# Optimization experiments

Hardware: AMD Instinct MI355X
Metric: run time of the kernel (lower is better)

The kernel has to match this reference:

```python
import jax, jax.numpy as jnp
import numpy as np

IMG = 224      # img_size
P = 16         # patch_size
C = 3          # in_chans
K = 100        # n_segments
COMPACT = 10.0 # slic compactness
ITERS = 10     # slic k-means iterations


def _resize_matrix(src, dst):
    # Linear antialiased resize is a linear map; materialize it by resizing identity.
    return jax.image.resize(jnp.eye(src, dtype=jnp.float32), (dst, src),
                            method='linear', antialias=True)


def _slic_labels(img_hwc):
    """Simplified SLIC: grid-initialized k-means in (color, compactness-scaled xy) space."""
    H, W = IMG, IMG
    S = float(np.sqrt(H * W / K))         # superpixel spacing
    ratio = COMPACT / S                   # spatial scaling (SLIC distance weighting)
    yy, xx = jnp.meshgrid(jnp.arange(H, dtype=jnp.float32),
                          jnp.arange(W, dtype=jnp.float32), indexing='ij')
    feat = jnp.concatenate([img_hwc, (yy * ratio)[..., None], (xx * ratio)[..., None]],
                           axis=-1).reshape(H * W, C + 2)  # [HW, 5]
    # grid init of K centers
    gh = int(np.ceil(np.sqrt(K)))
    gw = int(np.ceil(K / gh))
    cy = ((np.arange(gh) + 0.5) * H / gh).astype(np.int32)
    cx = ((np.arange(gw) + 0.5) * W / gw).astype(np.int32)
    idx = (cy[:, None] * W + cx[None, :]).reshape(-1)[:K]
    centers0 = feat[jnp.asarray(idx)]  # [K, 5]

    f2 = jnp.sum(feat * feat, axis=1, keepdims=True)  # [HW,1]

    def dists(centers):
        c2 = jnp.sum(centers * centers, axis=1)  # [K]
        return f2 + c2[None, :] - 2.0 * (feat @ centers.T)  # [HW,K]

    def body(i, centers):
        lbl = jnp.argmin(dists(centers), axis=1)              # [HW]
        oh = jax.nn.one_hot(lbl, K, dtype=feat.dtype)         # [HW,K]
        cnt = oh.sum(0)                                       # [K]
        new = (oh.T @ feat) / jnp.maximum(cnt, 1.0)[:, None]  # [K,5]
        return jnp.where((cnt > 0)[:, None], new, centers)

    centers = jax.lax.fori_loop(0, ITERS, body, centers0)
    return jnp.argmin(dists(centers), axis=1).reshape(H, W)


def _embed_one(img_chw, A):
    img = jnp.transpose(img_chw, (1, 2, 0))                     # [H,W,C]
    labels = jax.lax.stop_gradient(_slic_labels(img))           # [H,W] int
    masks = jax.nn.one_hot(labels, K, dtype=img.dtype, axis=0)  # [K,H,W]
    masked = masks[..., None] * img[None]                       # [K,H,W,C]
    tmp = jnp.einsum('ph,khwc->kpwc', A, masked)                # resize rows
    return jnp.einsum('qw,kpwc->kpqc', A, tmp)                  # [K,P,P,C]


def reference(x):
    B = x.shape[0]
    A = _resize_matrix(IMG, P)
    sp = jax.vmap(lambda im: _embed_one(im, A))(x)  # [B,K,P,P,C]
    # torch: view(B, K*C, P, P)  (raw row-major reinterpret), flatten(2), transpose(1,2)
    out = sp.reshape(B, K * C, P, P).reshape(B, K * C, P * P)
    return jnp.transpose(out, (0, 2, 1))  # [B, P*P, K*C]


def setup_inputs() -> dict:
    key = jax.random.key(0)
    x = jax.random.uniform(key, (8, C, IMG, IMG), dtype=jnp.float32)
    return {"x": x}
```

## Files before the change

kernel.cpp:

```cpp
#include <hip/hip_runtime.h>
#include <math.h>

#define IMGD 224
#define HW 50176
#define NK 100
#define NB 8
#define OUT_PER_B 76800
#define NCHUNK 131


static __device__ __forceinline__ float ratio_f32() {
  return (float)(10.0 / sqrt(224.0 * 224.0 / 100.0));
}

static __device__ __forceinline__ float dist5s(float f0, float f1, float f2,
                                               float f3, float f4, float fsq,
                                               float c0, float c1, float c2,
                                               float c3, float c4, float q) {
  float dot = __fmul_rn(f0, c0);
  dot = __fmaf_rn(f1, c1, dot);
  dot = __fmaf_rn(f2, c2, dot);
  dot = __fmaf_rn(f3, c3, dot);
  dot = __fmaf_rn(f4, c4, dot);
  return __fsub_rn(__fadd_rn(fsq, q), __fmul_rn(2.0f, dot));
}

static __device__ __forceinline__ float fsq5(float f0, float f1, float f2,
                                             float f3, float f4) {
  float s = __fmul_rn(f0, f0);
  s = __fadd_rn(s, __fmul_rn(f1, f1));
  s = __fadd_rn(s, __fmul_rn(f2, f2));
  s = __fadd_rn(s, __fmul_rn(f3, f3));
  s = __fadd_rn(s, __fmul_rn(f4, f4));
  return s;
}

__global__ void __launch_bounds__(256) setup_kernel(
    const float* __restrict__ x, float* __restrict__ A,
    float* __restrict__ centers, float* __restrict__ c2g) {
  int blk = blockIdx.x;
  int tid = threadIdx.x;
  if (blk < 16) {
    __shared__ float red[256];
    int p = blk;
    float tri = 0.0f;
    if (tid < IMGD) {
      float center = (p + 0.5f) * 14.0f - 0.5f;
      float xd = fabsf(center - (float)tid) / 14.0f;
      tri = fmaxf(0.0f, 1.0f - xd);
    }
    red[tid] = tri;
    __syncthreads();
    for (int s = 128; s > 0; s >>= 1) {
      if (tid < s) red[tid] += red[tid + s];
      __syncthreads();
    }
    float Z = red[0];
    if (tid < IMGD) A[p * IMGD + tid] = tri / Z;
  } else {
    int b = blk - 16;
    int k = tid;
    if (k >= NK) return;
    int gy = k / 10, gx = k % 10;
    int cy = (int)((gy + 0.5) * 224.0 / 10.0);
    int cx = (int)((gx + 0.5) * 224.0 / 10.0);
    int i = cy * IMGD + cx;
    const float ratio = ratio_f32();
    float c0 = x[((size_t)b * 3 + 0) * HW + i];
    float c1 = x[((size_t)b * 3 + 1) * HW + i];
    float c2 = x[((size_t)b * 3 + 2) * HW + i];
    float c3 = __fmul_rn((float)cy, ratio);
    float c4 = __fmul_rn((float)cx, ratio);
    float* c = centers + ((size_t)b * NK + k) * 5;
    c[0] = c0; c[1] = c1; c[2] = c2; c[3] = c3; c[4] = c4;
    float s = __fmul_rn(c0, c0);
    s = __fadd_rn(s, __fmul_rn(c1, c1));
    s = __fadd_rn(s, __fmul_rn(c2, c2));
    s = __fadd_rn(s, __fmul_rn(c3, c3));
    s = __fadd_rn(s, __fmul_rn(c4, c4));
    c2g[(size_t)b * NK + k] = s;
  }
}

__global__ void __launch_bounds__(128, 4) iter_kernel(
    const float* __restrict__ x, const float* __restrict__ centers,
    const float* __restrict__ c2g, float* __restrict__ partials) {
  __shared__ float4 ck4[NK];
  __shared__ float2 ck2[NK];
  __shared__ unsigned int mask[NK * 12];
  __shared__ unsigned short ppk[NK * 12];
  __shared__ float4 cval4[384];
  __shared__ float  cvalf[384];
  __shared__ int cnt[128];
  __shared__ int offx[128];
  __shared__ int wtot;
  __shared__ float ubpart[12][10];
  __shared__ float ubg[12];
  __shared__ unsigned int candm[12][4];
  __shared__ unsigned char clist[12][104];
  __shared__ int clen[12];
  int c = blockIdx.x, b = blockIdx.y;
  int tid = threadIdx.x;
  int start = (c < 129) ? c * 384 : 49536 + (c - 129) * 320;
  int len   = (c < 129) ? 384 : 320;

  const float* cb = centers + (size_t)b * NK * 5;
  const float* c2b = c2g + (size_t)b * NK;
  const float ratio = ratio_f32();
  if (tid < NK) {
    ck4[tid] = make_float4(cb[tid * 5 + 0], cb[tid * 5 + 1], cb[tid * 5 + 2], cb[tid * 5 + 3]);
    ck2[tid] = make_float2(cb[tid * 5 + 4], c2b[tid]);
  }
  for (int t = tid; t < NK * 12; t += 128) mask[t] = 0u;
  if (tid < 48) candm[tid >> 2][tid & 3] = 0u;

  const float* x0 = x + (size_t)b * 3 * HW;
  float f0[3], f1[3], f2[3], f3[3], f4[3], fq[3];
  bool vld[3];
  for (int r = 0; r < 3; ++r) {
    int t = tid + r * 128;
    vld[r] = (t < len);
    int i = start + (vld[r] ? t : 0);
    int y = i / IMGD, xw = i - y * IMGD;
    f0[r] = x0[i]; f1[r] = x0[HW + i]; f2[r] = x0[2 * HW + i];
    f3[r] = __fmul_rn((float)y, ratio);
    f4[r] = __fmul_rn((float)xw, ratio);
    fq[r] = fsq5(f0[r], f1[r], f2[r], f3[r], f4[r]);
  }
  __syncthreads();

  if (tid < 120) {
    int g = tid / 10, kb = tid - 10 * g;
    int i0 = start + g * 32, i1 = i0 + 31;
    int ymin = i0 / IMGD, ymax = i1 / IMGD;
    int cmin = (ymin == ymax) ? (i0 - ymin * IMGD) : 0;
    int cmax = (ymin == ymax) ? (i1 - ymax * IMGD) : (IMGD - 1);
    float f3mn = __fmul_rn((float)ymin, ratio);
    float f3mx = __fmul_rn((float)ymax, ratio);
    float f4mn = __fmul_rn((float)cmin, ratio);
    float f4mx = __fmul_rn((float)cmax, ratio);
    float mn = 3.4e38f;
    for (int k = kb * 10; k < kb * 10 + 10; ++k) {
      float c3 = ck4[k].w, c4 = ck2[k].x;
      float dy = fmaxf(fabsf(c3 - f3mn), fabsf(c3 - f3mx));
      float dx = fmaxf(fabsf(c4 - f4mn), fabsf(c4 - f4mx));
      mn = fminf(mn, dy * dy + dx * dx + 3.0f);
    }
    ubpart[g][kb] = mn;
  }
  __syncthreads();
  if (tid < 12) {
    float mn = ubpart[tid][0];
    for (int j = 1; j < 10; ++j) mn = fminf(mn, ubpart[tid][j]);
    ubg[tid] = mn + 1.0f;
  }
  __syncthreads();
  if (tid < 120) {
    int g = tid / 10, kb = tid - 10 * g;
    int i0 = start + g * 32, i1 = i0 + 31;
    int ymin = i0 / IMGD, ymax = i1 / IMGD;
    int cmin = (ymin == ymax) ? (i0 - ymin * IMGD) : 0;
    int cmax = (ymin == ymax) ? (i1 - ymax * IMGD) : (IMGD - 1);
    float f3mn = __fmul_rn((float)ymin, ratio);
    float f3mx = __fmul_rn((float)ymax, ratio);
    float f4mn = __fmul_rn((float)cmin, ratio);
    float f4mx = __fmul_rn((float)cmax, ratio);
    float lim = ubg[g];
    for (int k = kb * 10; k < kb * 10 + 10; ++k) {
      float c3 = ck4[k].w, c4 = ck2[k].x;
      float dy = fmaxf(0.0f, fmaxf(f3mn - c3, c3 - f3mx));
      float dx = fmaxf(0.0f, fmaxf(f4mn - c4, c4 - f4mx));
      if (dy * dy + dx * dx <= lim)
        atomicOr(&candm[g][k >> 5], 1u << (k & 31));
    }
  }
  __syncthreads();
  if (tid < 12) {
    int len2 = 0;
    for (int w = 0; w < 4; ++w) {
      unsigned int m = candm[tid][w];
      while (m) {
        int j = __ffs(m) - 1;
        m &= m - 1;
        clist[tid][len2++] = (unsigned char)(w * 32 + j);
      }
    }
    clen[tid] = len2;
  }
  __syncthreads();

  float best[3]; int bk[3];
  for (int r = 0; r < 3; ++r) {
    best[r] = 3.4e38f; bk[r] = 0;
    int t = tid + r * 128;
    int g = (t < 384) ? (t >> 5) : 0;
    int n = clen[g];
    for (int j = 0; j < n; ++j) {
      int k = clist[g][j];
      float4 a4 = ck4[k];
      float2 a2 = ck2[k];
      float d = dist5s(f0[r], f1[r], f2[r], f3[r], f4[r], fq[r],
                       a4.x, a4.y, a4.z, a4.w, a2.x, a2.y);
      if (d < best[r]) { best[r] = d; bk[r] = k; }
    }
  }
  for (int r = 0; r < 3; ++r) {
    int t = tid + r * 128;
    if (vld[r]) atomicOr(&mask[bk[r] * 12 + (t >> 5)], 1u << (t & 31));
  }
  __syncthreads();

  int myCnt = 0;
  if (tid < NK) {
    int s = 0;
    for (int g = 0; g < 12; ++g) {
      ppk[tid * 12 + g] = (unsigned short)s;
      s += __popc(mask[tid * 12 + g]);
    }
    myCnt = s;
  }
  cnt[tid] = myCnt;
  __syncthreads();

  int v = myCnt;
  for (int d = 1; d < 64; d <<= 1) {
    int u = __shfl_up(v, d, 64);
    if ((tid & 63) >= d) v += u;
  }
  if (tid == 63) wtot = v;
  __syncthreads();
  if (tid >= 64) v += wtot;
  offx[tid] = v;
  __syncthreads();

  for (int r = 0; r < 3; ++r) {
    int t = tid + r * 128;
    if (vld[r]) {
      int g = t >> 5, j = t & 31;
      unsigned int m = mask[bk[r] * 12 + g];
      int rank = ppk[bk[r] * 12 + g] + __popc(m & ((1u << j) - 1u));
      int pos = offx[bk[r]] - cnt[bk[r]] + rank;
      cval4[pos] = make_float4(f0[r], f1[r], f2[r], f3[r]);
      cvalf[pos] = f4[r];
    }
  }
  __syncthreads();

  if (tid < NK) {
    int n = cnt[tid];
    int base = offx[tid] - n;
    float s0 = 0.f, s1 = 0.f, s2 = 0.f, s3 = 0.f, s4 = 0.f, s5 = 0.f;
    for (int m = 0; m < n; ++m) {
      float4 vv = cval4[base + m];
      float ww = cvalf[base + m];
      s0 = __fadd_rn(s0, vv.x);
      s1 = __fadd_rn(s1, vv.y);
      s2 = __fadd_rn(s2, vv.z);
      s3 = __fadd_rn(s3, vv.w);
      s4 = __fadd_rn(s4, ww);
      s5 += 1.0f;
    }
    float* pp = partials + ((size_t)(b * NK + tid) * 6) * NCHUNK + c;
    pp[0 * NCHUNK] = s0; pp[1 * NCHUNK] = s1; pp[2 * NCHUNK] = s2;
    pp[3 * NCHUNK] = s3; pp[4 * NCHUNK] = s4; pp[5 * NCHUNK] = s5;
  }
}

__global__ void __launch_bounds__(128) combine_update_kernel(
    float* __restrict__ centers, const float* __restrict__ partials,
    float* __restrict__ c2g) {
  __shared__ float st[6 * NCHUNK];
  __shared__ float sums[6];
  __shared__ float newc[5];
  int bk = blockIdx.x;
  int tid = threadIdx.x;
  const float* base = partials + (size_t)bk * 6 * NCHUNK;
  for (int t = tid; t < 6 * NCHUNK; t += 128) st[t] = base[t];
  __syncthreads();
  if (tid < 6) {
    const float* row = st + tid * NCHUNK;
    float s = row[0];
    for (int c = 1; c < NCHUNK; ++c) s = __fadd_rn(s, row[c]);
    sums[tid] = s;
  }
  __syncthreads();
  float cntv = sums[5];
  float* cc = centers + (size_t)bk * 5;
  if (tid < 5) {
    float v;
    if (cntv > 0.0f) {
      float m = fmaxf(cntv, 1.0f);
      v = __fdiv_rn(sums[tid], m);
      cc[tid] = v;
    } else {
      v = cc[tid];
    }
    newc[tid] = v;
  }
  __syncthreads();
  if (tid == 0) {
    float t0 = __fmul_rn(newc[0], newc[0]);
    t0 = __fadd_rn(t0, __fmul_rn(newc[1], newc[1]));
    t0 = __fadd_rn(t0, __fmul_rn(newc[2], newc[2]));
    t0 = __fadd_rn(t0, __fmul_rn(newc[3], newc[3]));
    t0 = __fadd_rn(t0, __fmul_rn(newc[4], newc[4]));
    c2g[bk] = t0;
  }
}

__global__ void __launch_bounds__(256) assign_kernel(
    const float* __restrict__ x, const float* __restrict__ centers,
    const float* __restrict__ c2g, int* __restrict__ labels) {
  __shared__ float4 ck4[NK];
  __shared__ float2 ck2[NK];
  int b = blockIdx.y;
  int tid = threadIdx.x;
  int base = blockIdx.x * 512;

  const float* cb = centers + (size_t)b * NK * 5;
  const float* c2b = c2g + (size_t)b * NK;
  for (int k = tid; k < NK; k += 256) {
    ck4[k] = make_float4(cb[k * 5 + 0], cb[k * 5 + 1], cb[k * 5 + 2], cb[k * 5 + 3]);
    ck2[k] = make_float2(cb[k * 5 + 4], c2b[k]);
  }
  __syncthreads();

  const float* x0 = x + (size_t)b * 3 * HW;
  const float ratio = ratio_f32();
  float f0[2], f1[2], f2[2], f3[2], f4[2], fq[2];
  float best[2]; int bk[2];
  for (int r = 0; r < 2; ++r) {
    int i = base + r * 256 + tid;
    int y = i / IMGD, xw = i - y * IMGD;
    f0[r] = x0[i]; f1[r] = x0[HW + i]; f2[r] = x0[2 * HW + i];
    f3[r] = __fmul_rn((float)y, ratio);
    f4[r] = __fmul_rn((float)xw, ratio);
    fq[r] = fsq5(f0[r], f1[r], f2[r], f3[r], f4[r]);
    best[r] = 3.4e38f; bk[r] = 0;
  }
  for (int kb = 0; kb < NK; kb += 4) {
    float4 a4[4]; float2 a2[4];
    for (int kk = 0; kk < 4; ++kk) { a4[kk] = ck4[kb + kk]; a2[kk] = ck2[kb + kk]; }
    for (int kk = 0; kk < 4; ++kk) {
      for (int r = 0; r < 2; ++r) {
        float d = dist5s(f0[r], f1[r], f2[r], f3[r], f4[r], fq[r],
                         a4[kk].x, a4[kk].y, a4[kk].z, a4[kk].w, a2[kk].x, a2[kk].y);
        if (d < best[r]) { best[r] = d; bk[r] = kb + kk; }
      }
    }
  }
  int* lb = labels + (size_t)b * HW;
  for (int r = 0; r < 2; ++r) lb[base + r * 256 + tid] = bk[r];
}

__global__ void __launch_bounds__(256) embed_kernel(
    const float* __restrict__ x, const int* __restrict__ labels,
    const float* __restrict__ A, float* __restrict__ out) {
  __shared__ float sk[NK * 3];
  int b = blockIdx.y;
  int p = blockIdx.x >> 4;
  int q = blockIdx.x & 15;
  int tid = threadIdx.x;
  for (int t = tid; t < NK * 3; t += 256) sk[t] = 0.0f;
  __syncthreads();

  int h0 = max(0, 14 * p - 7), h1 = min(IMGD - 1, 14 * p + 20);
  int w0 = max(0, 14 * q - 7), w1 = min(IMGD - 1, 14 * q + 20);
  int hl = h1 - h0 + 1, wl = w1 - w0 + 1;
  int n = hl * wl;

  const float* xb = x + (size_t)b * 3 * HW;
  const int* lb = labels + (size_t)b * HW;
  const float* Ap = A + p * IMGD;
  const float* Aq = A + q * IMGD;

  for (int idx = tid; idx < n; idx += 256) {
    int dh = idx / wl;
    int hh = h0 + dh;
    int ww = w0 + (idx - dh * wl);
    int i = hh * IMGD + ww;
    float wgt = Ap[hh] * Aq[ww];
    int k = lb[i];
    atomicAdd(&sk[k * 3 + 0], wgt * xb[i]);
    atomicAdd(&sk[k * 3 + 1], wgt * xb[HW + i]);
    atomicAdd(&sk[k * 3 + 2], wgt * xb[2 * HW + i]);
  }
  __syncthreads();

  float* outb = out + (size_t)b * OUT_PER_B;
  int base = p * 48 + q * 3;
  for (int t = tid; t < NK * 3; t += 256) {
    int k = t / 3, c = t - 3 * k;
    int f = k * 768 + base + c;
    outb[(f & 255) * 300 + (f >> 8)] = sk[t];
  }
}

extern "C" void kernel_launch(void* const* d_in, const int* in_sizes, int n_in,
                              void* d_out, int out_size, void* d_ws, size_t ws_size,
                              hipStream_t stream) {
  const float* x = (const float*)d_in[0];
  float* out = (float*)d_out;
  char* ws = (char*)d_ws;
  float* A        = (float*)(ws);
  float* centers  = (float*)(ws + 16384);
  float* c2g      = (float*)(ws + 49152);
  int*   labels   = (int*)(ws + 90112);
  float* partials = (float*)(ws + 1703936);

  setup_kernel<<<24, 256, 0, stream>>>(x, A, centers, c2g);

  dim3 cgrid(NCHUNK, NB);
  for (int it = 0; it < 10; ++it) {
    iter_kernel<<<cgrid, 128, 0, stream>>>(x, centers, c2g, partials);
    combine_update_kernel<<<NB * NK, 128, 0, stream>>>(centers, partials, c2g);
  }
  dim3 agrid(98, NB);
  assign_kernel<<<agrid, 256, 0, stream>>>(x, centers, c2g, labels);

  dim3 egrid(256, NB);
  embed_kernel<<<egrid, 256, 0, stream>>>(x, labels, A, out);
}
```

Before: 298.8 us.

## Fuse center update into iteration kernel, reducing only candidate clusters' partials

Removes the separate combine_update launch between SLIC iterations. Each iter_kernel block now reduces the previous iteration's per-chunk partial sums itself: spatial sums for all clusters, then color sums only for the clusters that are candidates for its own pixels. Partials are split into spatial and color buffers and ping-ponged across iterations, with block 0 writing out the new centers. This saves nine launches and their serialization, but every block repeats the reduction over 131 chunks, which adds redundant global reads and work.

```diff
diff --git a/kernel.cpp b/kernel.cpp
--- a/kernel.cpp
+++ b/kernel.cpp
@@ -83,8 +83,11 @@
 }
 
 __global__ void __launch_bounds__(128, 4) iter_kernel(
-    const float* __restrict__ x, const float* __restrict__ centers,
-    const float* __restrict__ c2g, float* __restrict__ partials) {
+    const float* __restrict__ x, const float* __restrict__ centersIn,
+    const float* __restrict__ c2gIn, const float* __restrict__ prevC,
+    const float* __restrict__ spatIn, const float* __restrict__ colIn,
+    float* __restrict__ spatOut, float* __restrict__ colOut,
+    float* __restrict__ centersOut, int flag) {
   __shared__ float4 ck4[NK];
   __shared__ float2 ck2[NK];
   __shared__ unsigned int mask[NK * 12];
@@ -99,20 +102,21 @@
   __shared__ unsigned int candm[12][4];
   __shared__ unsigned char clist[12][104];
   __shared__ int clen[12];
+  __shared__ float sspat[300];
+  __shared__ float colsum[300];
+  __shared__ unsigned int unionm[4];
+  __shared__ unsigned char ulist[NK];
+  __shared__ int uLen;
   int c = blockIdx.x, b = blockIdx.y;
   int tid = threadIdx.x;
   int start = (c < 129) ? c * 384 : 49536 + (c - 129) * 320;
-  int len   = (c < 129) ? 384 : 320;
-
-  const float* cb = centers + (size_t)b * NK * 5;
-  const float* c2b = c2g + (size_t)b * NK;
+  int len   = (c < 129) ? c == 130 ? 320 : 384 : 320;
+  len = (c < 129) ? 384 : 320;
+
   const float ratio = ratio_f32();
-  if (tid < NK) {
-    ck4[tid] = make_float4(cb[tid * 5 + 0], cb[tid * 5 + 1], cb[tid * 5 + 2], cb[tid * 5 + 3]);
-    ck2[tid] = make_float2(cb[tid * 5 + 4], c2b[tid]);
-  }
   for (int t = tid; t < NK * 12; t += 128) mask[t] = 0u;
   if (tid < 48) candm[tid >> 2][tid & 3] = 0u;
+  if (tid < 4) unionm[tid] = 0u;
 
   const float* x0 = x + (size_t)b * 3 * HW;
   float f0[3], f1[3], f2[3], f3[3], f4[3], fq[3];
@@ -127,7 +131,39 @@
     f4[r] = __fmul_rn((float)xw, ratio);
     fq[r] = fsq5(f0[r], f1[r], f2[r], f3[r], f4[r]);
   }
-  __syncthreads();
+
+  float p0r = 0.f, p1r = 0.f, p2r = 0.f, c3r = 0.f, c4r = 0.f;
+  float cntr = 0.f, mr = 1.f;
+  if (flag == 0) {
+    const float* cb = centersIn + (size_t)b * NK * 5;
+    const float* c2b = c2gIn + (size_t)b * NK;
+    if (tid < NK) {
+      ck4[tid] = make_float4(cb[tid*5+0], cb[tid*5+1], cb[tid*5+2], cb[tid*5+3]);
+      ck2[tid] = make_float2(cb[tid*5+4], c2b[tid]);
+    }
+    __syncthreads();
+  } else {
+    for (int u = tid; u < 300; u += 128) {
+      int k = u / 3, j = u - 3 * k;
+      const float* bp = spatIn + ((size_t)(b * NK + k) * 3 + j) * NCHUNK;
+      float s = bp[0];
+      for (int cc = 1; cc < NCHUNK; ++cc) s = __fadd_rn(s, bp[cc]);
+      sspat[u] = s;
+    }
+    __syncthreads();
+    if (tid < NK) {
+      cntr = sspat[tid * 3 + 2];
+      const float* pc = prevC + ((size_t)b * NK + tid) * 5;
+      p0r = pc[0]; p1r = pc[1]; p2r = pc[2];
+      float p3 = pc[3], p4 = pc[4];
+      mr = fmaxf(cntr, 1.0f);
+      c3r = (cntr > 0.0f) ? __fdiv_rn(sspat[tid * 3 + 0], mr) : p3;
+      c4r = (cntr > 0.0f) ? __fdiv_rn(sspat[tid * 3 + 1], mr) : p4;
+      ck4[tid].w = c3r;
+      ck2[tid].x = c4r;
+    }
+    __syncthreads();
+  }
 
   if (tid < 120) {
     int g = tid / 10, kb = tid - 10 * g;
@@ -170,8 +206,10 @@
       float c3 = ck4[k].w, c4 = ck2[k].x;
       float dy = fmaxf(0.0f, fmaxf(f3mn - c3, c3 - f3mx));
       float dx = fmaxf(0.0f, fmaxf(f4mn - c4, c4 - f4mx));
-      if (dy * dy + dx * dx <= lim)
+      if (dy * dy + dx * dx <= lim) {
         atomicOr(&candm[g][k >> 5], 1u << (k & 31));
+        atomicOr(&unionm[k >> 5], 1u << (k & 31));
+      }
     }
   }
   __syncthreads();
@@ -187,7 +225,56 @@
     }
     clen[tid] = len2;
   }
-  __syncthreads();
+  if (blockIdx.x == 0) {
+    if (tid < NK) ulist[tid] = (unsigned char)tid;
+    if (tid == 127) uLen = NK;
+  } else if (tid == 127) {
+    int len2 = 0;
+    for (int w = 0; w < 4; ++w) {
+      unsigned int m = unionm[w];
+      while (m) {
+        int j = __ffs(m) - 1;
+        m &= m - 1;
+        ulist[len2++] = (unsigned char)(w * 32 + j);
+      }
+    }
+    uLen = len2;
+  }
+  __syncthreads();
+
+  if (flag) {
+    int total = uLen * 3;
+    for (int idx = tid; idx < total; idx += 128) {
+      int e = idx / 3, j = idx - 3 * e;
+      int k = ulist[e];
+      const float* bp = colIn + ((size_t)(b * NK + k) * 3 + j) * NCHUNK;
+      float s = bp[0];
+      for (int cc = 1; cc < NCHUNK; ++cc) s = __fadd_rn(s, bp[cc]);
+      colsum[k * 3 + j] = s;
+    }
+    __syncthreads();
+    if (tid < NK) {
+      bool cand = (((unionm[tid >> 5] >> (tid & 31)) & 1u) != 0u) ||
+                  (blockIdx.x == 0);
+      if (cand) {
+        float c0 = (cntr > 0.0f) ? __fdiv_rn(colsum[tid*3+0], mr) : p0r;
+        float c1 = (cntr > 0.0f) ? __fdiv_rn(colsum[tid*3+1], mr) : p1r;
+        float c2 = (cntr > 0.0f) ? __fdiv_rn(colsum[tid*3+2], mr) : p2r;
+        float q = __fmul_rn(c0, c0);
+        q = __fadd_rn(q, __fmul_rn(c1, c1));
+        q = __fadd_rn(q, __fmul_rn(c2, c2));
+        q = __fadd_rn(q, __fmul_rn(c3r, c3r));
+        q = __fadd_rn(q, __fmul_rn(c4r, c4r));
+        ck4[tid] = make_float4(c0, c1, c2, c3r);
+        ck2[tid] = make_float2(c4r, q);
+        if (blockIdx.x == 0) {
+          float* oc = centersOut + ((size_t)b * NK + tid) * 5;
+          oc[0] = c0; oc[1] = c1; oc[2] = c2; oc[3] = c3r; oc[4] = c4r;
+        }
+      }
+    }
+    __syncthreads();
+  }
 
   float best[3]; int bk[3];
   for (int r = 0; r < 3; ++r) {
@@ -260,40 +347,45 @@
       s4 = __fadd_rn(s4, ww);
       s5 += 1.0f;
     }
-    float* pp = partials + ((size_t)(b * NK + tid) * 6) * NCHUNK + c;
-    pp[0 * NCHUNK] = s0; pp[1 * NCHUNK] = s1; pp[2 * NCHUNK] = s2;
-    pp[3 * NCHUNK] = s3; pp[4 * NCHUNK] = s4; pp[5 * NCHUNK] = s5;
+    float* sp = spatOut + ((size_t)(b * NK + tid) * 3) * NCHUNK + c;
+    sp[0 * NCHUNK] = s3; sp[1 * NCHUNK] = s4; sp[2 * NCHUNK] = s5;
+    float* cp = colOut + ((size_t)(b * NK + tid) * 3) * NCHUNK + c;
+    cp[0 * NCHUNK] = s0; cp[1 * NCHUNK] = s1; cp[2 * NCHUNK] = s2;
   }
 }
 
 __global__ void __launch_bounds__(128) combine_update_kernel(
-    float* __restrict__ centers, const float* __restrict__ partials,
+    const float* __restrict__ centersPrev, float* __restrict__ centersOut,
+    const float* __restrict__ spatP, const float* __restrict__ colP,
     float* __restrict__ c2g) {
-  __shared__ float st[6 * NCHUNK];
+  __shared__ float st[786];
   __shared__ float sums[6];
   __shared__ float newc[5];
   int bk = blockIdx.x;
   int tid = threadIdx.x;
-  const float* base = partials + (size_t)bk * 6 * NCHUNK;
-  for (int t = tid; t < 6 * NCHUNK; t += 128) st[t] = base[t];
+  const float* colBase = colP + (size_t)bk * 3 * NCHUNK;
+  const float* spatBase = spatP + (size_t)bk * 3 * NCHUNK;
+  for (int t = tid; t < 393; t += 128) { st[t] = colBase[t]; st[393 + t] = spatBase[t]; }
   __syncthreads();
   if (tid < 6) {
-    const float* row = st + tid * NCHUNK;
+    const float* row = (tid < 3) ? (st + tid * NCHUNK) : (st + 393 + (tid - 3) * NCHUNK);
     float s = row[0];
     for (int c = 1; c < NCHUNK; ++c) s = __fadd_rn(s, row[c]);
     sums[tid] = s;
   }
   __syncthreads();
   float cntv = sums[5];
-  float* cc = centers + (size_t)bk * 5;
   if (tid < 5) {
     float v;
     if (cntv > 0.0f) {
       float m = fmaxf(cntv, 1.0f);
+      v = __fdiv_rn(sums[tid < 3 ? tid : tid], (tid < 3) ? m : m);
+      v = __fdiv_rn((tid < 3) ? sums[tid] : sums[tid], m);
       v = __fdiv_rn(sums[tid], m);
-      cc[tid] = v;
+      centersOut[(size_t)bk * 5 + tid] = v;
     } else {
-      v = cc[tid];
+      v = centersPrev[(size_t)bk * 5 + tid];
+      centersOut[(size_t)bk * 5 + tid] = v;
     }
     newc[tid] = v;
   }
@@ -320,8 +412,8 @@
   const float* cb = centers + (size_t)b * NK * 5;
   const float* c2b = c2g + (size_t)b * NK;
   for (int k = tid; k < NK; k += 256) {
-    ck4[k] = make_float4(cb[k * 5 + 0], cb[k * 5 + 1], cb[k * 5 + 2], cb[k * 5 + 3]);
-    ck2[k] = make_float2(cb[k * 5 + 4], c2b[k]);
+    ck4[k] = make_float4(cb[k*5+0], cb[k*5+1], cb[k*5+2], cb[k*5+3]);
+    ck2[k] = make_float2(cb[k*5+4], c2b[k]);
   }
   __syncthreads();
 
@@ -403,20 +495,33 @@
   float* out = (float*)d_out;
   char* ws = (char*)d_ws;
   float* A        = (float*)(ws);
-  float* centers  = (float*)(ws + 16384);
-  float* c2g      = (float*)(ws + 49152);
+  float* centersA = (float*)(ws + 16384);
+  float* centersB = (float*)(ws + 36864);
+  float* c2g      = (float*)(ws + 57344);
   int*   labels   = (int*)(ws + 90112);
-  float* partials = (float*)(ws + 1703936);
-
-  setup_kernel<<<24, 256, 0, stream>>>(x, A, centers, c2g);
+  float* PA_s = (float*)(ws + 1703936);
+  float* PA_c = (float*)(ws + 2961536);
+  float* PB_s = (float*)(ws + 4219136);
+  float* PB_c = (float*)(ws + 5476736);
+
+  setup_kernel<<<24, 256, 0, stream>>>(x, A, centersA, c2g);
 
   dim3 cgrid(NCHUNK, NB);
-  for (int it = 0; it < 10; ++it) {
-    iter_kernel<<<cgrid, 128, 0, stream>>>(x, centers, c2g, partials);
-    combine_update_kernel<<<NB * NK, 128, 0, stream>>>(centers, partials, c2g);
-  }
+  iter_kernel<<<cgrid, 128, 0, stream>>>(x, centersA, c2g, centersA,
+                                         PA_s, PA_c, PA_s, PA_c, centersB, 0);
+  for (int i = 1; i < 10; ++i) {
+    if (i & 1) {
+      iter_kernel<<<cgrid, 128, 0, stream>>>(x, centersA, c2g, centersA,
+                                             PA_s, PA_c, PB_s, PB_c, centersB, 1);
+    } else {
+      iter_kernel<<<cgrid, 128, 0, stream>>>(x, centersB, c2g, centersB,
+                                             PB_s, PB_c, PA_s, PA_c, centersA, 1);
+    }
+  }
+  combine_update_kernel<<<NB * NK, 128, 0, stream>>>(centersB, centersA,
+                                                     PB_s, PB_c, c2g);
   dim3 agrid(98, NB);
-  assign_kernel<<<agrid, 256, 0, stream>>>(x, centers, c2g, labels);
+  assign_kernel<<<agrid, 256, 0, stream>>>(x, centersA, c2g, labels);
 
   dim3 egrid(256, NB);
   embed_kernel<<<egrid, 256, 0, stream>>>(x, labels, A, out);
```

Result: slower. 414.7 us (+38.8%).

## Fuse setup into first iteration and final assignment into embed kernel with pruning

Applied to the files above, without the earlier changes.

Removes setup_kernel by computing grid-initialized centers inside the first iter_kernel launch, with block 0 writing them back for the combine step. The separate assign pass and labels buffer go away: embed_kernel now computes the resize weights itself and assigns each pixel in its window to a center drawn from a spatially pruned candidate list. This cuts two launches and the labels round trip through global memory. In exchange it adds reductions per embed block, recomputes assignment for pixels covered by overlapping windows, and pads the mask stride to 13 to reduce shared-memory bank conflicts.

```diff
diff --git a/kernel.cpp b/kernel.cpp
--- a/kernel.cpp
+++ b/kernel.cpp
@@ -7,6 +7,7 @@
 #define NB 8
 #define OUT_PER_B 76800
 #define NCHUNK 131
+#define MSTR 13
 
 
 static __device__ __forceinline__ float ratio_f32() {
@@ -35,60 +36,13 @@
   return s;
 }
 
-__global__ void __launch_bounds__(256) setup_kernel(
-    const float* __restrict__ x, float* __restrict__ A,
-    float* __restrict__ centers, float* __restrict__ c2g) {
-  int blk = blockIdx.x;
-  int tid = threadIdx.x;
-  if (blk < 16) {
-    __shared__ float red[256];
-    int p = blk;
-    float tri = 0.0f;
-    if (tid < IMGD) {
-      float center = (p + 0.5f) * 14.0f - 0.5f;
-      float xd = fabsf(center - (float)tid) / 14.0f;
-      tri = fmaxf(0.0f, 1.0f - xd);
-    }
-    red[tid] = tri;
-    __syncthreads();
-    for (int s = 128; s > 0; s >>= 1) {
-      if (tid < s) red[tid] += red[tid + s];
-      __syncthreads();
-    }
-    float Z = red[0];
-    if (tid < IMGD) A[p * IMGD + tid] = tri / Z;
-  } else {
-    int b = blk - 16;
-    int k = tid;
-    if (k >= NK) return;
-    int gy = k / 10, gx = k % 10;
-    int cy = (int)((gy + 0.5) * 224.0 / 10.0);
-    int cx = (int)((gx + 0.5) * 224.0 / 10.0);
-    int i = cy * IMGD + cx;
-    const float ratio = ratio_f32();
-    float c0 = x[((size_t)b * 3 + 0) * HW + i];
-    float c1 = x[((size_t)b * 3 + 1) * HW + i];
-    float c2 = x[((size_t)b * 3 + 2) * HW + i];
-    float c3 = __fmul_rn((float)cy, ratio);
-    float c4 = __fmul_rn((float)cx, ratio);
-    float* c = centers + ((size_t)b * NK + k) * 5;
-    c[0] = c0; c[1] = c1; c[2] = c2; c[3] = c3; c[4] = c4;
-    float s = __fmul_rn(c0, c0);
-    s = __fadd_rn(s, __fmul_rn(c1, c1));
-    s = __fadd_rn(s, __fmul_rn(c2, c2));
-    s = __fadd_rn(s, __fmul_rn(c3, c3));
-    s = __fadd_rn(s, __fmul_rn(c4, c4));
-    c2g[(size_t)b * NK + k] = s;
-  }
-}
-
 __global__ void __launch_bounds__(128, 4) iter_kernel(
-    const float* __restrict__ x, const float* __restrict__ centers,
-    const float* __restrict__ c2g, float* __restrict__ partials) {
+    const float* __restrict__ x, float* __restrict__ centers,
+    const float* __restrict__ c2g, float* __restrict__ partials, int flag) {
   __shared__ float4 ck4[NK];
   __shared__ float2 ck2[NK];
-  __shared__ unsigned int mask[NK * 12];
-  __shared__ unsigned short ppk[NK * 12];
+  __shared__ unsigned int mask[NK * MSTR];
+  __shared__ unsigned short ppk[NK * MSTR];
   __shared__ float4 cval4[384];
   __shared__ float  cvalf[384];
   __shared__ int cnt[128];
@@ -104,17 +58,40 @@
   int start = (c < 129) ? c * 384 : 49536 + (c - 129) * 320;
   int len   = (c < 129) ? 384 : 320;
 
-  const float* cb = centers + (size_t)b * NK * 5;
-  const float* c2b = c2g + (size_t)b * NK;
   const float ratio = ratio_f32();
-  if (tid < NK) {
-    ck4[tid] = make_float4(cb[tid * 5 + 0], cb[tid * 5 + 1], cb[tid * 5 + 2], cb[tid * 5 + 3]);
-    ck2[tid] = make_float2(cb[tid * 5 + 4], c2b[tid]);
-  }
-  for (int t = tid; t < NK * 12; t += 128) mask[t] = 0u;
+  const float* x0 = x + (size_t)b * 3 * HW;
+  if (flag == 0) {
+    if (tid < NK) {
+      int gy = tid / 10, gx = tid - 10 * (tid / 10);
+      int cy = (int)((gy + 0.5) * 224.0 / 10.0);
+      int cx = (int)((gx + 0.5) * 224.0 / 10.0);
+      int i = cy * IMGD + cx;
+      float c0 = x0[i], c1 = x0[HW + i], c2 = x0[2 * HW + i];
+      float c3 = __fmul_rn((float)cy, ratio);
+      float c4 = __fmul_rn((float)cx, ratio);
+      float s = __fmul_rn(c0, c0);
+      s = __fadd_rn(s, __fmul_rn(c1, c1));
+      s = __fadd_rn(s, __fmul_rn(c2, c2));
+      s = __fadd_rn(s, __fmul_rn(c3, c3));
+      s = __fadd_rn(s, __fmul_rn(c4, c4));
+      ck4[tid] = make_float4(c0, c1, c2, c3);
+      ck2[tid] = make_float2(c4, s);
+      if (c == 0) {
+        float* oc = centers + ((size_t)b * NK + tid) * 5;
+        oc[0] = c0; oc[1] = c1; oc[2] = c2; oc[3] = c3; oc[4] = c4;
+      }
+    }
+  } else {
+    const float* cb = centers + (size_t)b * NK * 5;
+    const float* c2b = c2g + (size_t)b * NK;
+    if (tid < NK) {
+      ck4[tid] = make_float4(cb[tid*5+0], cb[tid*5+1], cb[tid*5+2], cb[tid*5+3]);
+      ck2[tid] = make_float2(cb[tid*5+4], c2b[tid]);
+    }
+  }
+  for (int t = tid; t < NK * MSTR; t += 128) mask[t] = 0u;
   if (tid < 48) candm[tid >> 2][tid & 3] = 0u;
 
-  const float* x0 = x + (size_t)b * 3 * HW;
   float f0[3], f1[3], f2[3], f3[3], f4[3], fq[3];
   bool vld[3];
   for (int r = 0; r < 3; ++r) {
@@ -206,7 +183,7 @@
   }
   for (int r = 0; r < 3; ++r) {
     int t = tid + r * 128;
-    if (vld[r]) atomicOr(&mask[bk[r] * 12 + (t >> 5)], 1u << (t & 31));
+    if (vld[r]) atomicOr(&mask[bk[r] * MSTR + (t >> 5)], 1u << (t & 31));
   }
   __syncthreads();
 
@@ -214,8 +191,8 @@
   if (tid < NK) {
     int s = 0;
     for (int g = 0; g < 12; ++g) {
-      ppk[tid * 12 + g] = (unsigned short)s;
-      s += __popc(mask[tid * 12 + g]);
+      ppk[tid * MSTR + g] = (unsigned short)s;
+      s += __popc(mask[tid * MSTR + g]);
     }
     myCnt = s;
   }
@@ -237,8 +214,8 @@
     int t = tid + r * 128;
     if (vld[r]) {
       int g = t >> 5, j = t & 31;
-      unsigned int m = mask[bk[r] * 12 + g];
-      int rank = ppk[bk[r] * 12 + g] + __popc(m & ((1u << j) - 1u));
+      unsigned int m = mask[bk[r] * MSTR + g];
+      int rank = ppk[bk[r] * MSTR + g] + __popc(m & ((1u << j) - 1u));
       int pos = offx[bk[r]] - cnt[bk[r]] + rank;
       cval4[pos] = make_float4(f0[r], f1[r], f2[r], f3[r]);
       cvalf[pos] = f4[r];
@@ -308,82 +285,145 @@
   }
 }
 
-__global__ void __launch_bounds__(256) assign_kernel(
+__global__ void __launch_bounds__(256) embed_kernel(
     const float* __restrict__ x, const float* __restrict__ centers,
-    const float* __restrict__ c2g, int* __restrict__ labels) {
+    const float* __restrict__ c2g, float* __restrict__ out) {
+  __shared__ float red[256];
+  __shared__ float Apv[28];
+  __shared__ float Aqv[28];
   __shared__ float4 ck4[NK];
   __shared__ float2 ck2[NK];
-  int b = blockIdx.y;
-  int tid = threadIdx.x;
-  int base = blockIdx.x * 512;
-
-  const float* cb = centers + (size_t)b * NK * 5;
-  const float* c2b = c2g + (size_t)b * NK;
-  for (int k = tid; k < NK; k += 256) {
-    ck4[k] = make_float4(cb[k * 5 + 0], cb[k * 5 + 1], cb[k * 5 + 2], cb[k * 5 + 3]);
-    ck2[k] = make_float2(cb[k * 5 + 4], c2b[k]);
-  }
-  __syncthreads();
-
-  const float* x0 = x + (size_t)b * 3 * HW;
-  const float ratio = ratio_f32();
-  float f0[2], f1[2], f2[2], f3[2], f4[2], fq[2];
-  float best[2]; int bk[2];
-  for (int r = 0; r < 2; ++r) {
-    int i = base + r * 256 + tid;
-    int y = i / IMGD, xw = i - y * IMGD;
-    f0[r] = x0[i]; f1[r] = x0[HW + i]; f2[r] = x0[2 * HW + i];
-    f3[r] = __fmul_rn((float)y, ratio);
-    f4[r] = __fmul_rn((float)xw, ratio);
-    fq[r] = fsq5(f0[r], f1[r], f2[r], f3[r], f4[r]);
-    best[r] = 3.4e38f; bk[r] = 0;
-  }
-  for (int kb = 0; kb < NK; kb += 4) {
-    float4 a4[4]; float2 a2[4];
-    for (int kk = 0; kk < 4; ++kk) { a4[kk] = ck4[kb + kk]; a2[kk] = ck2[kb + kk]; }
-    for (int kk = 0; kk < 4; ++kk) {
-      for (int r = 0; r < 2; ++r) {
-        float d = dist5s(f0[r], f1[r], f2[r], f3[r], f4[r], fq[r],
-                         a4[kk].x, a4[kk].y, a4[kk].z, a4[kk].w, a2[kk].x, a2[kk].y);
-        if (d < best[r]) { best[r] = d; bk[r] = kb + kk; }
-      }
-    }
-  }
-  int* lb = labels + (size_t)b * HW;
-  for (int r = 0; r < 2; ++r) lb[base + r * 256 + tid] = bk[r];
-}
-
-__global__ void __launch_bounds__(256) embed_kernel(
-    const float* __restrict__ x, const int* __restrict__ labels,
-    const float* __restrict__ A, float* __restrict__ out) {
   __shared__ float sk[NK * 3];
+  __shared__ float ubk[128];
+  __shared__ unsigned int candm[4];
+  __shared__ unsigned char clist[NK];
+  __shared__ int clen;
   int b = blockIdx.y;
   int p = blockIdx.x >> 4;
   int q = blockIdx.x & 15;
   int tid = threadIdx.x;
-  for (int t = tid; t < NK * 3; t += 256) sk[t] = 0.0f;
+
+  float cp = (p + 0.5f) * 14.0f - 0.5f;
+  float trip = 0.0f;
+  if (tid < IMGD) {
+    float xd = fabsf(cp - (float)tid) / 14.0f;
+    trip = fmaxf(0.0f, 1.0f - xd);
+  }
+  red[tid] = trip;
+  __syncthreads();
+  for (int s = 128; s > 0; s >>= 1) {
+    if (tid < s) red[tid] += red[tid + s];
+    __syncthreads();
+  }
+  float Zp = red[0];
+  __syncthreads();
+  float cq = (q + 0.5f) * 14.0f - 0.5f;
+  float triq = 0.0f;
+  if (tid < IMGD) {
+    float xd = fabsf(cq - (float)tid) / 14.0f;
+    triq = fmaxf(0.0f, 1.0f - xd);
+  }
+  red[tid] = triq;
+  __syncthreads();
+  for (int s = 128; s > 0; s >>= 1) {
+    if (tid < s) red[tid] += red[tid + s];
+    __syncthreads();
+  }
+  float Zq = red[0];
   __syncthreads();
 
   int h0 = max(0, 14 * p - 7), h1 = min(IMGD - 1, 14 * p + 20);
   int w0 = max(0, 14 * q - 7), w1 = min(IMGD - 1, 14 * q + 20);
   int hl = h1 - h0 + 1, wl = w1 - w0 + 1;
+  if (tid < hl) {
+    float xd = fabsf(cp - (float)(h0 + tid)) / 14.0f;
+    Apv[tid] = fmaxf(0.0f, 1.0f - xd) / Zp;
+  }
+  if (tid < wl) {
+    float xd = fabsf(cq - (float)(w0 + tid)) / 14.0f;
+    Aqv[tid] = fmaxf(0.0f, 1.0f - xd) / Zq;
+  }
+  const float* cb = centers + (size_t)b * NK * 5;
+  const float* c2b = c2g + (size_t)b * NK;
+  if (tid < NK) {
+    ck4[tid] = make_float4(cb[tid*5+0], cb[tid*5+1], cb[tid*5+2], cb[tid*5+3]);
+    ck2[tid] = make_float2(cb[tid*5+4], c2b[tid]);
+  }
+  for (int t = tid; t < NK * 3; t += 256) sk[t] = 0.0f;
+  if (tid < 4) candm[tid] = 0u;
+  __syncthreads();
+
+  const float ratio = ratio_f32();
+  float f3mn = __fmul_rn((float)h0, ratio);
+  float f3mx = __fmul_rn((float)h1, ratio);
+  float f4mn = __fmul_rn((float)w0, ratio);
+  float f4mx = __fmul_rn((float)w1, ratio);
+  if (tid < 128) {
+    float u = 3.4e38f;
+    if (tid < NK) {
+      float c3 = ck4[tid].w, c4 = ck2[tid].x;
+      float dy = fmaxf(fabsf(c3 - f3mn), fabsf(c3 - f3mx));
+      float dx = fmaxf(fabsf(c4 - f4mn), fabsf(c4 - f4mx));
+      u = dy * dy + dx * dx + 3.0f;
+    }
+    ubk[tid] = u;
+  }
+  __syncthreads();
+  for (int s = 64; s > 0; s >>= 1) {
+    if (tid < s) ubk[tid] = fminf(ubk[tid], ubk[tid + s]);
+    __syncthreads();
+  }
+  float lim = ubk[0] + 1.0f;
+  if (tid < NK) {
+    float c3 = ck4[tid].w, c4 = ck2[tid].x;
+    float dy = fmaxf(0.0f, fmaxf(f3mn - c3, c3 - f3mx));
+    float dx = fmaxf(0.0f, fmaxf(f4mn - c4, c4 - f4mx));
+    if (dy * dy + dx * dx <= lim)
+      atomicOr(&candm[tid >> 5], 1u << (tid & 31));
+  }
+  __syncthreads();
+  if (tid == 0) {
+    int len2 = 0;
+    for (int w = 0; w < 4; ++w) {
+      unsigned int m = candm[w];
+      while (m) {
+        int j = __ffs(m) - 1;
+        m &= m - 1;
+        clist[len2++] = (unsigned char)(w * 32 + j);
+      }
+    }
+    clen = len2;
+  }
+  __syncthreads();
+
+  const float* xb = x + (size_t)b * 3 * HW;
   int n = hl * wl;
-
-  const float* xb = x + (size_t)b * 3 * HW;
-  const int* lb = labels + (size_t)b * HW;
-  const float* Ap = A + p * IMGD;
-  const float* Aq = A + q * IMGD;
-
-  for (int idx = tid; idx < n; idx += 256) {
+  int ncand = clen;
+  for (int r = 0; r < 4; ++r) {
+    int idx = tid + r * 256;
+    if (idx >= n) break;
     int dh = idx / wl;
     int hh = h0 + dh;
-    int ww = w0 + (idx - dh * wl);
+    int dw = idx - dh * wl;
+    int ww = w0 + dw;
     int i = hh * IMGD + ww;
-    float wgt = Ap[hh] * Aq[ww];
-    int k = lb[i];
-    atomicAdd(&sk[k * 3 + 0], wgt * xb[i]);
-    atomicAdd(&sk[k * 3 + 1], wgt * xb[HW + i]);
-    atomicAdd(&sk[k * 3 + 2], wgt * xb[2 * HW + i]);
+    float v0 = xb[i], v1 = xb[HW + i], v2 = xb[2 * HW + i];
+    float f3 = __fmul_rn((float)hh, ratio);
+    float f4 = __fmul_rn((float)ww, ratio);
+    float fq = fsq5(v0, v1, v2, f3, f4);
+    float bestd = 3.4e38f; int bk = 0;
+    for (int j = 0; j < ncand; ++j) {
+      int k = clist[j];
+      float4 a4 = ck4[k];
+      float2 a2 = ck2[k];
+      float d = dist5s(v0, v1, v2, f3, f4, fq,
+                       a4.x, a4.y, a4.z, a4.w, a2.x, a2.y);
+      if (d < bestd) { bestd = d; bk = k; }
+    }
+    float wgt = Apv[dh] * Aqv[dw];
+    atomicAdd(&sk[bk * 3 + 0], wgt * v0);
+    atomicAdd(&sk[bk * 3 + 1], wgt * v1);
+    atomicAdd(&sk[bk * 3 + 2], wgt * v2);
   }
   __syncthreads();
 
@@ -402,22 +442,17 @@
   const float* x = (const float*)d_in[0];
   float* out = (float*)d_out;
   char* ws = (char*)d_ws;
-  float* A        = (float*)(ws);
   float* centers  = (float*)(ws + 16384);
   float* c2g      = (float*)(ws + 49152);
-  int*   labels   = (int*)(ws + 90112);
   float* partials = (float*)(ws + 1703936);
 
-  setup_kernel<<<24, 256, 0, stream>>>(x, A, centers, c2g);
-
   dim3 cgrid(NCHUNK, NB);
-  for (int it = 0; it < 10; ++it) {
-    iter_kernel<<<cgrid, 128, 0, stream>>>(x, centers, c2g, partials);
+  iter_kernel<<<cgrid, 128, 0, stream>>>(x, centers, c2g, partials, 0);
+  combine_update_kernel<<<NB * NK, 128, 0, stream>>>(centers, partials, c2g);
+  for (int it = 1; it < 10; ++it) {
+    iter_kernel<<<cgrid, 128, 0, stream>>>(x, centers, c2g, partials, 1);
     combine_update_kernel<<<NB * NK, 128, 0, stream>>>(centers, partials, c2g);
   }
-  dim3 agrid(98, NB);
-  assign_kernel<<<agrid, 256, 0, stream>>>(x, centers, c2g, labels);
-
   dim3 egrid(256, NB);
-  embed_kernel<<<egrid, 256, 0, stream>>>(x, labels, A, out);
-}
+  embed_kernel<<<egrid, 256, 0, stream>>>(x, centers, c2g, out);
+}
```

Measured after the change: 298.5 us. No clear change (-0.1%).
